# Performance work log

Hardware: AMD Instinct MI355X
Metric: run time of the kernel (lower is better)

## Reference

```python
import jax, jax.numpy as jnp
import numpy as np

RATIO, DS = 0.4, 4.0  # resolution, downsample_rate
B_, L_, C_, H_, W_ = 2, 4, 128, 96, 96


def get_transformation_matrix(M, H, W):
    # kornia-style rotation about image center: T = shift @ R @ shift_inv, then add translation
    R = M[..., :2, :2]
    center = jnp.array([W / 2.0, H / 2.0], jnp.float32)
    t = center - jnp.einsum('...ij,j->...i', R, center) + M[..., :, 2]
    return jnp.concatenate([R, t[..., None]], axis=-1)  # (...,2,3)


def _grid_sample(img, grid):
    # img (N,C,H,W), grid (N,H,W,2) normalized; bilinear, zeros padding, align_corners=True
    N, C, H, W = img.shape
    gx = (grid[..., 0] + 1.0) * 0.5 * (W - 1)
    gy = (grid[..., 1] + 1.0) * 0.5 * (H - 1)
    x0 = jnp.floor(gx); y0 = jnp.floor(gy)
    wx = gx - x0; wy = gy - y0

    def one(im, x0, y0, wx, wy):
        def samp(xi, yi):
            valid = ((xi >= 0) & (xi <= W - 1) & (yi >= 0) & (yi <= H - 1)).astype(im.dtype)
            xc = jnp.clip(xi, 0, W - 1).astype(jnp.int32)
            yc = jnp.clip(yi, 0, H - 1).astype(jnp.int32)
            return im[:, yc, xc] * valid[None]
        return (samp(x0, y0) * (1 - wx) * (1 - wy) + samp(x0 + 1, y0) * wx * (1 - wy)
                + samp(x0, y0 + 1) * (1 - wx) * wy + samp(x0 + 1, y0 + 1) * wx * wy)

    return jax.vmap(one)(img, x0, y0, wx, wy)


def warp_affine(src, M, H, W):
    # torch F.affine_grid + grid_sample with normalized homography (align_corners=True)
    n = jnp.array([[2.0 / (W - 1), 0.0, -1.0],
                   [0.0, 2.0 / (H - 1), -1.0],
                   [0.0, 0.0, 1.0]], jnp.float32)
    bottom = jnp.broadcast_to(jnp.array([[0.0, 0.0, 1.0]], jnp.float32), M.shape[:-2] + (1, 3))
    Mh = jnp.concatenate([M, bottom], axis=-2)
    theta = jnp.linalg.inv(n @ Mh @ jnp.linalg.inv(n))[..., :2, :]
    xs = jnp.linspace(-1.0, 1.0, W); ys = jnp.linspace(-1.0, 1.0, H)
    gx, gy = jnp.meshgrid(xs, ys)  # (H,W)
    pts = jnp.stack([gx, gy, jnp.ones_like(gx)], -1)
    grid = jnp.einsum('nij,hwj->nhwi', theta, pts)
    return _grid_sample(src, grid)


def _forward(x, record_len, pairwise_t_matrix, w1, b1, s1, t1, w2, b2, s2, t2,
             w3, b3, s3, t3, w4, b4, mlp_w, mlp_b):
    _, C, H, W = x.shape
    B, L = pairwise_t_matrix.shape[:2]
    N = L  # regular grouping: record_len[b] == L for all b
    feats = x.reshape(B, N, C, H, W)

    # get_discretized_transformation_matrix: rows [0,1], cols [0,1,3]; translation / (ratio*ds)
    tm = pairwise_t_matrix[..., :2, :][..., jnp.array([0, 1, 3])]  # (B,L,L,2,3)
    tm = jnp.concatenate([tm[..., :2], tm[..., 2:] / (RATIO * DS)], axis=-1)

    # get_rotated_roi: warp all-ones maps by the pairwise transforms
    roi = warp_affine(jnp.ones((B * L * L, 1, H, W), x.dtype),
                      get_transformation_matrix(tm.reshape(-1, 2, 3), H, W), H, W)
    roi = roi.reshape(B, L, L, 1, H, W)

    # rearrange 'b c h w -> b c w h' then flip last axis
    f = jnp.flip(jnp.swapaxes(feats, -1, -2), axis=-1)  # (B,N,C,H,W), H==W
    is_first = jnp.zeros((B, N), bool).at[0, 0].set(True)  # first_frame flag -> (b=0,i=0)
    ch = jnp.arange(C)

    def pwf(h):
        # PixelWeightedFusionSoftmax trunk: 1x1 convs + inference BN (folded scale/shift) + relu
        def layer(h, w, b, s, t):
            h = jnp.einsum('nchw,oc->nohw', h, w) + b[:, None, None]
            return jax.nn.relu(h * s[:, None, None] + t[:, None, None])
        h = layer(h, w1, b1, s1, t1)
        h = layer(h, w2, b2, s2, t2)
        h = layer(h, w3, b3, s3, t3)
        return jax.nn.relu(jnp.einsum('nchw,oc->nohw', h, w4) + b4[:, None, None])  # (N,1,H,W)

    def per_target(f_b, tm_i, roi_i, ego_f, first):
        # f_b (N,C,H,W); tm_i (N,2,3); roi_i (N,1,H,W); ego_f (C,H,W)
        T = get_transformation_matrix(tm_i, H, W)
        neighbor = warp_affine(f_b, T, H, W)               # (N,C,H,W)
        ego = jnp.broadcast_to(ego_f[None], neighbor.shape)
        # process_features: replace top-k (k=1; k=C for the very first pair) std channels
        std = jnp.std(ego_f, axis=(1, 2), ddof=1)          # per-channel std (unbiased)
        chan_mask = (ch == jnp.argmax(std))[None, :, None, None]
        sel = jnp.where(first, neighbor, jnp.where(chan_mask, neighbor, ego))
        logits = pwf(jnp.concatenate([sel, ego], axis=1))  # (N,1,H,W)
        logits = jnp.where(roi_i == 0, -jnp.inf, logits)
        wgt = jax.nn.softmax(logits, axis=0)               # softmax over agents
        out = (wgt * sel * roi_i).sum(0)                   # (C,H,W)
        return jnp.swapaxes(jnp.flip(out, axis=-1), -1, -2)  # undo flip + rearrange

    def per_batch(f_b, tm_b, roi_b, first_b):
        return jax.vmap(per_target, in_axes=(None, 1, 1, 0, 0))(f_b, tm_b, roi_b, f_b, first_b)

    updated = jax.vmap(per_batch)(f, tm, roi, is_first)    # (B,N,C,H,W)
    out = jnp.transpose(updated[:, 0], (0, 2, 3, 1))       # ego agent, (B,H,W,C)
    return out @ mlp_w.T + mlp_b


def setup_inputs() -> dict:
    key = jax.random.key(0)
    ks = jax.random.split(key, 20)
    B, L, C, H, W = B_, L_, C_, H_, W_
    x = jax.random.normal(ks[0], (B * L, C, H, W), jnp.float32)
    record_len = jnp.full((B,), L, jnp.int32)

    # near-identity SE(2) pairwise transforms (exact identity on diagonal)
    ang = jax.random.uniform(ks[1], (B, L, L), minval=-0.1, maxval=0.1)
    tr = jax.random.uniform(ks[2], (B, L, L, 2), minval=-2.0, maxval=2.0)
    eye = jnp.eye(L, dtype=bool)[None]
    ang = jnp.where(eye, 0.0, ang)
    tr = jnp.where(eye[..., None], 0.0, tr)
    c, s = jnp.cos(ang), jnp.sin(ang)
    P = jnp.zeros((B, L, L, 4, 4), jnp.float32)
    P = P.at[..., 0, 0].set(c).at[..., 0, 1].set(-s).at[..., 1, 0].set(s).at[..., 1, 1].set(c)
    P = P.at[..., 2, 2].set(1.0).at[..., 3, 3].set(1.0)
    P = P.at[..., 0, 3].set(tr[..., 0]).at[..., 1, 3].set(tr[..., 1])

    def winit(k, o, i):
        return jax.random.normal(k, (o, i), jnp.float32) / np.sqrt(i).astype(np.float32)

    inp = dict(x=x, record_len=record_len, pairwise_t_matrix=P,
               w1=winit(ks[3], 128, 2 * C), b1=jnp.zeros(128, jnp.float32),
               s1=1.0 + 0.1 * jax.random.normal(ks[4], (128,), jnp.float32),
               t1=0.1 * jax.random.normal(ks[5], (128,), jnp.float32),
               w2=winit(ks[6], 32, 128), b2=jnp.zeros(32, jnp.float32),
               s2=1.0 + 0.1 * jax.random.normal(ks[7], (32,), jnp.float32),
               t2=0.1 * jax.random.normal(ks[8], (32,), jnp.float32),
               w3=winit(ks[9], 8, 32), b3=jnp.zeros(8, jnp.float32),
               s3=1.0 + 0.1 * jax.random.normal(ks[10], (8,), jnp.float32),
               t3=0.1 * jax.random.normal(ks[11], (8,), jnp.float32),
               w4=winit(ks[12], 1, 8), b4=jnp.zeros(1, jnp.float32),
               mlp_w=winit(ks[13], C, C),
               mlp_b=0.01 * jax.random.normal(ks[14], (C,), jnp.float32))
    return inp


def reference(x, record_len, pairwise_t_matrix, w1, b1, s1, t1, w2, b2, s2, t2,
              w3, b3, s3, t3, w4, b4, mlp_w, mlp_b):
    return _forward(x, record_len, pairwise_t_matrix, w1, b1, s1, t1, w2, b2, s2, t2,
                    w3, b3, s3, t3, w4, b4, mlp_w, mlp_b)
```

## Files before the change

kernel.cpp:

```cpp
#include <hip/hip_runtime.h>
#include <hip/hip_bf16.h>
#include <math.h>

#define HW 9216
#define CC 128

typedef __attribute__((ext_vector_type(4))) float f32x4;
typedef __attribute__((ext_vector_type(8))) short s16x8;

static __device__ __forceinline__ unsigned short f2bf(float f) {
    __hip_bfloat16 h = __float2bfloat16(f);
    return *reinterpret_cast<unsigned short*>(&h);
}
static __device__ __forceinline__ float bf2f(unsigned short u) {
    unsigned int v = ((unsigned int)u) << 16;
    float f;
    __builtin_memcpy(&f, &v, 4);
    return f;
}

__global__ void k_theta(const float* __restrict__ P, float* __restrict__ th) {
    int t = threadIdx.x;
    if (t >= 8) return;
    int b = t >> 2, j = t & 3;
    const float* M = P + (size_t)(b * 4 + j) * 64;
    float a00 = M[0], a01 = M[1], a02 = M[3] / 1.6f;
    float a10 = M[4], a11 = M[5], a12 = M[7] / 1.6f;
    const float cx = 48.f, cy = 48.f;
    float T02 = cx - (a00 * cx + a01 * cy) + a02;
    float T12 = cy - (a10 * cx + a11 * cy) + a12;
    float A02 = a00 + a01 - 1.f + (2.f / 95.f) * T02;
    float A12 = a10 + a11 - 1.f + (2.f / 95.f) * T12;
    float det = a00 * a11 - a01 * a10;
    float i00 = a11 / det, i01 = -a01 / det, i10 = -a10 / det, i11 = a00 / det;
    float* o = th + t * 6;
    o[0] = i00; o[1] = i01; o[2] = -(i00 * A02 + i01 * A12);
    o[3] = i10; o[4] = i11; o[5] = -(i10 * A02 + i11 * A12);
}

__global__ __launch_bounds__(256) void k_wcvt(const float* __restrict__ w1, const float* __restrict__ w2,
                                              const float* __restrict__ mw,
                                              unsigned short* __restrict__ w1b, unsigned short* __restrict__ w2b,
                                              unsigned short* __restrict__ mwb) {
    int t = blockIdx.x * 256 + threadIdx.x;
    int nthr = gridDim.x * 256;
    for (int i = t; i < 32768; i += nthr) w1b[i] = f2bf(w1[i]);
    for (int i = t; i < 16384; i += nthr) mwb[i] = f2bf(mw[i]);
    if (t < 4096) w2b[t] = f2bf(w2[t]);
}

__global__ __launch_bounds__(256) void k_transpose(const float* __restrict__ x, unsigned short* __restrict__ xT) {
    int bn = blockIdx.x / 96, y = blockIdx.x % 96;
    __shared__ float tile[96][129];
    const float* src = x + (size_t)bn * 128 * HW + (size_t)y * 96;
    for (int i = threadIdx.x; i < 128 * 96; i += 256) {
        int c = i / 96, xx = i - c * 96;
        tile[xx][c] = src[(size_t)c * HW + xx];
    }
    __syncthreads();
    unsigned int* dst = (unsigned int*)(xT + ((size_t)bn * 96 + y) * 96 * 128);
    for (int i = threadIdx.x; i < 96 * 64; i += 256) {
        int xx = i >> 6, cp = i & 63;
        unsigned int pk = (unsigned int)f2bf(tile[xx][cp * 2]) | ((unsigned int)f2bf(tile[xx][cp * 2 + 1]) << 16);
        dst[xx * 64 + cp] = pk;
    }
}

__global__ __launch_bounds__(256) void k_var(const float* __restrict__ x, float* __restrict__ var) {
    int b = blockIdx.x >> 7, c = blockIdx.x & 127;
    const float* src = x + ((size_t)(b * 4) * 128 + c) * HW;
    float s = 0.f, ss = 0.f;
    for (int i = threadIdx.x; i < HW; i += 256) { float v = src[i]; s += v; ss += v * v; }
    __shared__ float rs[256], rss[256];
    rs[threadIdx.x] = s; rss[threadIdx.x] = ss; __syncthreads();
    for (int o = 128; o > 0; o >>= 1) {
        if (threadIdx.x < o) { rs[threadIdx.x] += rs[threadIdx.x + o]; rss[threadIdx.x] += rss[threadIdx.x + o]; }
        __syncthreads();
    }
    if (threadIdx.x == 0) {
        float mean = rs[0] / 9216.f;
        var[b * 128 + c] = (rss[0] - 9216.f * mean * mean) / 9215.f;
    }
}

__global__ void k_argmax(const float* __restrict__ var, int* __restrict__ cmax) {
    int b = blockIdx.x, t = threadIdx.x;
    __shared__ float v[128]; __shared__ int idx[128];
    v[t] = var[b * 128 + t]; idx[t] = t; __syncthreads();
    for (int o = 64; o > 0; o >>= 1) {
        if (t < o) { if (v[t + o] > v[t]) { v[t] = v[t + o]; idx[t] = idx[t + o]; } }
        __syncthreads();
    }
    if (t == 0) cmax[b] = idx[0];
}

__global__ __launch_bounds__(256) void k_gather(const unsigned short* __restrict__ xT, const float* __restrict__ th,
                                                const int* __restrict__ cmax, unsigned short* __restrict__ sel16,
                                                float* __restrict__ roi) {
    int blk = blockIdx.x;
    int bj6 = blk / 576, pblk = blk - bj6 * 576;
    int b = bj6 / 3, jm = bj6 - b * 3, j = jm + 1;
    int pr = threadIdx.x >> 7, c = threadIdx.x & 127;
    const float* t6 = th + (b * 4 + j) * 6;
    float T0 = t6[0], T1 = t6[1], T2 = t6[2], T3 = t6[3], T4 = t6[4], T5 = t6[5];
    int cm = cmax[b];
    const unsigned short* base = xT + (size_t)(b * 4 + j) * HW * CC;
    const unsigned short* ebase = xT + (size_t)(b * 4) * HW * CC;
    #pragma unroll
    for (int it = 0; it < 8; it++) {
        int p = pblk * 16 + it * 2 + pr;
        int h = p / 96, w = p - h * 96;
        float X = -1.f + (2.f / 95.f) * (float)w, Y = -1.f + (2.f / 95.f) * (float)h;
        float gx = T0 * X + T1 * Y + T2;
        float gy = T3 * X + T4 * Y + T5;
        float px = (gx + 1.f) * 47.5f, py = (gy + 1.f) * 47.5f;
        float x0f = floorf(px), y0f = floorf(py);
        float wx = px - x0f, wy = py - y0f;
        int x0 = (int)x0f, y0 = (int)y0f, x1 = x0 + 1, y1 = y0 + 1;
        float w00 = (1.f - wx) * (1.f - wy), w10 = wx * (1.f - wy);
        float w01 = (1.f - wx) * wy, w11 = wx * wy;
        bool vx0 = (x0 >= 0) && (x0 <= 95), vx1 = (x1 >= 0) && (x1 <= 95);
        bool vy0 = (y0 >= 0) && (y0 <= 95), vy1 = (y1 >= 0) && (y1 <= 95);
        float f00 = (vx0 && vy0) ? w00 : 0.f, f10 = (vx1 && vy0) ? w10 : 0.f;
        float f01 = (vx0 && vy1) ? w01 : 0.f, f11 = (vx1 && vy1) ? w11 : 0.f;
        int xc0 = min(max(x0, 0), 95), xc1 = min(max(x1, 0), 95);
        int yc0 = min(max(y0, 0), 95), yc1 = min(max(y1, 0), 95);
        float nb = f00 * bf2f(base[((95 - xc0) * 96 + yc0) * CC + c])
                 + f10 * bf2f(base[((95 - xc1) * 96 + yc0) * CC + c])
                 + f01 * bf2f(base[((95 - xc0) * 96 + yc1) * CC + c])
                 + f11 * bf2f(base[((95 - xc1) * 96 + yc1) * CC + c]);
        unsigned short egov = ebase[((95 - w) * 96 + h) * CC + c];
        unsigned short sv = (b == 0) ? f2bf(nb) : ((c == cm) ? f2bf(nb) : egov);
        sel16[((size_t)bj6 * HW + p) * CC + c] = sv;
        if (c == 0) roi[(size_t)bj6 * HW + p] = f00 + f10 + f01 + f11;
    }
}

__global__ __launch_bounds__(256) void k_fused(
    const unsigned short* __restrict__ xT, const unsigned short* __restrict__ sel16,
    const float* __restrict__ roiB,
    const unsigned short* __restrict__ w1b, const unsigned short* __restrict__ w2b,
    const unsigned short* __restrict__ mwb,
    const float* __restrict__ b1, const float* __restrict__ s1, const float* __restrict__ t1,
    const float* __restrict__ b2, const float* __restrict__ s2, const float* __restrict__ t2,
    const float* __restrict__ w3, const float* __restrict__ b3, const float* __restrict__ s3,
    const float* __restrict__ t3, const float* __restrict__ w4, const float* __restrict__ b4,
    const float* __restrict__ mb, float* __restrict__ out) {
    __shared__ __align__(16) unsigned char sm[47232];
    float* l2s  = (float*)(sm + 40960);
    float* lgs  = (float*)(sm + 45696);
    float* rois = (float*)(sm + 46208);
    float* wgt  = (float*)(sm + 46720);
    int t = threadIdx.x;
    int blk = blockIdx.x;
    int b = blk / 288, pt = blk - b * 288;
    int p0 = pt * 32;
    const unsigned short* egb = xT + (size_t)(b * 4) * HW * CC;
    #pragma unroll
    for (int it = 0; it < 2; it++) {
        int u = it * 256 + t;
        int px = u >> 4, g = u & 15;
        int p = p0 + px;
        int h = p / 96, w = p - h * 96;
        s16x8 v = *(const s16x8*)(egb + (size_t)((95 - w) * 96 + h) * CC + g * 8);
        *(s16x8*)(sm + px * 256 + ((g * 16) ^ ((px & 7) << 4))) = v;
    }
    #pragma unroll
    for (int j = 1; j < 4; j++) {
        const unsigned short* sp = sel16 + ((size_t)(b * 3 + j - 1) * HW + p0) * CC;
        #pragma unroll
        for (int it = 0; it < 2; it++) {
            int u = it * 256 + t;
            int px = u >> 4, g = u & 15;
            s16x8 v = *(const s16x8*)(sp + px * 128 + g * 8);
            *(s16x8*)(sm + j * 8192 + px * 256 + ((g * 16) ^ ((px & 7) << 4))) = v;
        }
    }
    if (t < 128) {
        int j = t >> 5, px = t & 31;
        rois[j * 32 + px] = (j == 0) ? 1.f : roiB[(size_t)(b * 3 + j - 1) * HW + p0 + px];
    }
    int lane = t & 63, w_ = t >> 6, l15 = lane & 15, l4 = lane >> 4;
    float bb[2], ss[2], tt[2];
    #pragma unroll
    for (int nt = 0; nt < 2; nt++) {
        int o = w_ * 32 + nt * 16 + l15;
        bb[nt] = b1[o]; ss[nt] = s1[o]; tt[nt] = t1[o];
    }
    int mt2 = w_ >> 1, nt2 = w_ & 1;
    float b2v, s2v, t2v;
    { int o2 = nt2 * 16 + l15; b2v = b2[o2]; s2v = s2[o2]; t2v = t2[o2]; }
    __syncthreads();
    for (int j = 0; j < 4; j++) {
        f32x4 acc[2][2];
        #pragma unroll
        for (int mt = 0; mt < 2; mt++)
            #pragma unroll
            for (int nt = 0; nt < 2; nt++) acc[mt][nt] = f32x4{0.f, 0.f, 0.f, 0.f};
        const unsigned char* selj = sm + j * 8192;
        #pragma unroll
        for (int kt = 0; kt < 8; kt++) {
            const unsigned char* src = (kt < 4) ? selj : sm;
            int kloc = (kt & 3) * 32 + l4 * 8;
            s16x8 bfr[2];
            #pragma unroll
            for (int nt = 0; nt < 2; nt++)
                bfr[nt] = *(const s16x8*)(w1b + (size_t)(w_ * 32 + nt * 16 + l15) * 256 + kt * 32 + l4 * 8);
            #pragma unroll
            for (int mt = 0; mt < 2; mt++) {
                int px = mt * 16 + l15;
                s16x8 af = *(const s16x8*)(src + px * 256 + ((2 * kloc) ^ ((px & 7) << 4)));
                #pragma unroll
                for (int nt = 0; nt < 2; nt++)
                    acc[mt][nt] = __builtin_amdgcn_mfma_f32_16x16x32_bf16(af, bfr[nt], acc[mt][nt], 0, 0, 0);
            }
        }
        __syncthreads();
        #pragma unroll
        for (int mt = 0; mt < 2; mt++) {
            #pragma unroll
            for (int nt = 0; nt < 2; nt++) {
                int o = w_ * 32 + nt * 16 + l15;
                #pragma unroll
                for (int r = 0; r < 4; r++) {
                    int px = mt * 16 + l4 * 4 + r;
                    float v = fmaxf((acc[mt][nt][r] + bb[nt]) * ss[nt] + tt[nt], 0.f);
                    *(unsigned short*)(sm + 32768 + px * 256 + ((2 * o) ^ ((px & 7) << 4))) = f2bf(v);
                }
            }
        }
        __syncthreads();
        f32x4 acc2 = f32x4{0.f, 0.f, 0.f, 0.f};
        {
            int px = mt2 * 16 + l15;
            #pragma unroll
            for (int kt = 0; kt < 4; kt++) {
                s16x8 af = *(const s16x8*)(sm + 32768 + px * 256 + ((2 * (kt * 32 + l4 * 8)) ^ ((px & 7) << 4)));
                s16x8 bf = *(const s16x8*)(w2b + (size_t)(nt2 * 16 + l15) * 128 + kt * 32 + l4 * 8);
                acc2 = __builtin_amdgcn_mfma_f32_16x16x32_bf16(af, bf, acc2, 0, 0, 0);
            }
        }
        {
            int o2 = nt2 * 16 + l15;
            #pragma unroll
            for (int r = 0; r < 4; r++) {
                int pxr = mt2 * 16 + l4 * 4 + r;
                l2s[pxr * 37 + o2] = fmaxf((acc2[r] + b2v) * s2v + t2v, 0.f);
            }
        }
        __syncthreads();
        if (t < 32) {
            int px = t;
            float xv[32];
            #pragma unroll
            for (int k = 0; k < 32; k++) xv[k] = l2s[px * 37 + k];
            float lg = b4[0];
            #pragma unroll
            for (int o = 0; o < 8; o++) {
                float a = 0.f;
                #pragma unroll
                for (int k = 0; k < 32; k++) a += xv[k] * w3[o * 32 + k];
                float l3v = fmaxf((a + b3[o]) * s3[o] + t3[o], 0.f);
                lg += w4[o] * l3v;
            }
            lgs[j * 32 + px] = fmaxf(lg, 0.f);
        }
    }
    __syncthreads();
    if (t < 32) {
        int px = t;
        float rr[4], lg[4];
        #pragma unroll
        for (int j = 0; j < 4; j++) { rr[j] = rois[j * 32 + px]; lg[j] = lgs[j * 32 + px]; }
        float m = -1e30f;
        #pragma unroll
        for (int j = 0; j < 4; j++) if (rr[j] != 0.f && lg[j] > m) m = lg[j];
        float e[4], se = 0.f;
        #pragma unroll
        for (int j = 0; j < 4; j++) { e[j] = (rr[j] != 0.f) ? expf(lg[j] - m) : 0.f; se += e[j]; }
        float inv = 1.f / se;
        #pragma unroll
        for (int j = 0; j < 4; j++) wgt[j * 32 + px] = e[j] * inv * rr[j];
    }
    __syncthreads();
    #pragma unroll
    for (int it = 0; it < 2; it++) {
        int u = it * 256 + t;
        int px = u >> 4, g = u & 15;
        int byo = (g * 16) ^ ((px & 7) << 4);
        float wj[4];
        #pragma unroll
        for (int j = 0; j < 4; j++) wj[j] = wgt[j * 32 + px];
        float accv[8];
        #pragma unroll
        for (int e = 0; e < 8; e++) accv[e] = 0.f;
        #pragma unroll
        for (int j = 0; j < 4; j++) {
            s16x8 v = *(const s16x8*)(sm + j * 8192 + px * 256 + byo);
            #pragma unroll
            for (int e = 0; e < 8; e++) accv[e] += wj[j] * bf2f((unsigned short)v[e]);
        }
        s16x8 pk;
        #pragma unroll
        for (int e = 0; e < 8; e++) pk[e] = (short)f2bf(accv[e]);
        *(s16x8*)(sm + 32768 + px * 256 + byo) = pk;
    }
    __syncthreads();
    f32x4 acc3[2][2];
    #pragma unroll
    for (int mt = 0; mt < 2; mt++)
        #pragma unroll
        for (int nt = 0; nt < 2; nt++) acc3[mt][nt] = f32x4{0.f, 0.f, 0.f, 0.f};
    #pragma unroll
    for (int kt = 0; kt < 4; kt++) {
        s16x8 bfr[2];
        #pragma unroll
        for (int nt = 0; nt < 2; nt++)
            bfr[nt] = *(const s16x8*)(mwb + (size_t)(w_ * 32 + nt * 16 + l15) * 128 + kt * 32 + l4 * 8);
        #pragma unroll
        for (int mt = 0; mt < 2; mt++) {
            int px = mt * 16 + l15;
            s16x8 af = *(const s16x8*)(sm + 32768 + px * 256 + ((kt * 64 + l4 * 16) ^ ((px & 7) << 4)));
            #pragma unroll
            for (int nt = 0; nt < 2; nt++)
                acc3[mt][nt] = __builtin_amdgcn_mfma_f32_16x16x32_bf16(af, bfr[nt], acc3[mt][nt], 0, 0, 0);
        }
    }
    float mbv[2];
    #pragma unroll
    for (int nt = 0; nt < 2; nt++) mbv[nt] = mb[w_ * 32 + nt * 16 + l15];
    #pragma unroll
    for (int mt = 0; mt < 2; mt++) {
        #pragma unroll
        for (int nt = 0; nt < 2; nt++) {
            #pragma unroll
            for (int r = 0; r < 4; r++) {
                int px = mt * 16 + l4 * 4 + r;
                int p = p0 + px;
                int h = p / 96, ww = p - h * 96;
                out[(((size_t)b * 96 + (95 - ww)) * 96 + h) * CC + w_ * 32 + nt * 16 + l15] = acc3[mt][nt][r] + mbv[nt];
            }
        }
    }
}

extern "C" void kernel_launch(void* const* d_in, const int* in_sizes, int n_in,
                              void* d_out, int out_size, void* d_ws, size_t ws_size,
                              hipStream_t stream) {
    const float* x  = (const float*)d_in[0];
    const float* P  = (const float*)d_in[2];
    const float* w1 = (const float*)d_in[3];
    const float* b1 = (const float*)d_in[4];
    const float* s1 = (const float*)d_in[5];
    const float* t1 = (const float*)d_in[6];
    const float* w2 = (const float*)d_in[7];
    const float* b2 = (const float*)d_in[8];
    const float* s2 = (const float*)d_in[9];
    const float* t2 = (const float*)d_in[10];
    const float* w3 = (const float*)d_in[11];
    const float* b3 = (const float*)d_in[12];
    const float* s3 = (const float*)d_in[13];
    const float* t3 = (const float*)d_in[14];
    const float* w4 = (const float*)d_in[15];
    const float* b4 = (const float*)d_in[16];
    const float* mw = (const float*)d_in[17];
    const float* mb = (const float*)d_in[18];
    float* out = (float*)d_out;

    float* ws = (float*)d_ws;
    float* TH  = ws;
    float* VAR = ws + 64;
    int*   CMX = (int*)(ws + 320);
    unsigned short* XT    = (unsigned short*)(ws + 384);
    unsigned short* SEL16 = XT + 9437184;
    float* ROI = (float*)(SEL16 + 7077888);
    unsigned short* W1B = (unsigned short*)(ROI + 55296);
    unsigned short* W2B = W1B + 32768;
    unsigned short* MWB = W2B + 4096;

    k_theta<<<1, 64, 0, stream>>>(P, TH);
    k_wcvt<<<32, 256, 0, stream>>>(w1, w2, mw, W1B, W2B, MWB);
    k_transpose<<<768, 256, 0, stream>>>(x, XT);
    k_var<<<256, 256, 0, stream>>>(x, VAR);
    k_argmax<<<2, 128, 0, stream>>>(VAR, CMX);
    k_gather<<<3456, 256, 0, stream>>>(XT, TH, CMX, SEL16, ROI);
    k_fused<<<576, 256, 0, stream>>>(XT, SEL16, ROI, W1B, W2B, MWB,
                                     b1, s1, t1, b2, s2, t2, w3, b3, s3, t3, w4, b4, mb, out);
}
```

Measured before the change: 185.9 us.

## Fuse variance into transpose, vectorize gather, restructure fused MLP per-wave

Merges the theta and weight-conversion kernels into one prep kernel. The per-channel variance is now computed inside the transpose kernel from the shared tile, with atomics into a zeroed buffer, which removes a separate full read of x. The gather kernel now loads 8 channels per thread with 16-byte vector loads instead of scalar bf16 loads. The fused kernel gives each wave its own agent j, so it computes all 128 outputs with per-wave scratch and no block-wide barriers between stages, and the weighted-sum stage is folded into the final MFMA A-operand load; in exchange shared memory grows to about 66 KB, which may reduce occupancy.

```diff
diff --git a/kernel.cpp b/kernel.cpp
--- a/kernel.cpp
+++ b/kernel.cpp
@@ -19,37 +19,37 @@
     return f;
 }
 
-__global__ void k_theta(const float* __restrict__ P, float* __restrict__ th) {
-    int t = threadIdx.x;
-    if (t >= 8) return;
-    int b = t >> 2, j = t & 3;
-    const float* M = P + (size_t)(b * 4 + j) * 64;
-    float a00 = M[0], a01 = M[1], a02 = M[3] / 1.6f;
-    float a10 = M[4], a11 = M[5], a12 = M[7] / 1.6f;
-    const float cx = 48.f, cy = 48.f;
-    float T02 = cx - (a00 * cx + a01 * cy) + a02;
-    float T12 = cy - (a10 * cx + a11 * cy) + a12;
-    float A02 = a00 + a01 - 1.f + (2.f / 95.f) * T02;
-    float A12 = a10 + a11 - 1.f + (2.f / 95.f) * T12;
-    float det = a00 * a11 - a01 * a10;
-    float i00 = a11 / det, i01 = -a01 / det, i10 = -a10 / det, i11 = a00 / det;
-    float* o = th + t * 6;
-    o[0] = i00; o[1] = i01; o[2] = -(i00 * A02 + i01 * A12);
-    o[3] = i10; o[4] = i11; o[5] = -(i10 * A02 + i11 * A12);
-}
-
-__global__ __launch_bounds__(256) void k_wcvt(const float* __restrict__ w1, const float* __restrict__ w2,
+__global__ __launch_bounds__(256) void k_prep(const float* __restrict__ P,
+                                              const float* __restrict__ w1, const float* __restrict__ w2,
                                               const float* __restrict__ mw,
+                                              float* __restrict__ th,
                                               unsigned short* __restrict__ w1b, unsigned short* __restrict__ w2b,
                                               unsigned short* __restrict__ mwb) {
     int t = blockIdx.x * 256 + threadIdx.x;
+    if (blockIdx.x == 0 && threadIdx.x < 8) {
+        int i = threadIdx.x;
+        const float* M = P + (size_t)i * 64;
+        float a00 = M[0], a01 = M[1], a02 = M[3] / 1.6f;
+        float a10 = M[4], a11 = M[5], a12 = M[7] / 1.6f;
+        const float cx = 48.f, cy = 48.f;
+        float T02 = cx - (a00 * cx + a01 * cy) + a02;
+        float T12 = cy - (a10 * cx + a11 * cy) + a12;
+        float A02 = a00 + a01 - 1.f + (2.f / 95.f) * T02;
+        float A12 = a10 + a11 - 1.f + (2.f / 95.f) * T12;
+        float det = a00 * a11 - a01 * a10;
+        float i00 = a11 / det, i01 = -a01 / det, i10 = -a10 / det, i11 = a00 / det;
+        float* o = th + i * 6;
+        o[0] = i00; o[1] = i01; o[2] = -(i00 * A02 + i01 * A12);
+        o[3] = i10; o[4] = i11; o[5] = -(i10 * A02 + i11 * A12);
+    }
     int nthr = gridDim.x * 256;
     for (int i = t; i < 32768; i += nthr) w1b[i] = f2bf(w1[i]);
     for (int i = t; i < 16384; i += nthr) mwb[i] = f2bf(mw[i]);
-    if (t < 4096) w2b[t] = f2bf(w2[t]);
-}
-
-__global__ __launch_bounds__(256) void k_transpose(const float* __restrict__ x, unsigned short* __restrict__ xT) {
+    for (int i = t; i < 4096; i += nthr) w2b[i] = f2bf(w2[i]);
+}
+
+__global__ __launch_bounds__(256) void k_transpose(const float* __restrict__ x, unsigned short* __restrict__ xT,
+                                                   float* __restrict__ vsum) {
     int bn = blockIdx.x / 96, y = blockIdx.x % 96;
     __shared__ float tile[96][129];
     const float* src = x + (size_t)bn * 128 * HW + (size_t)y * 96;
@@ -64,29 +64,24 @@
         unsigned int pk = (unsigned int)f2bf(tile[xx][cp * 2]) | ((unsigned int)f2bf(tile[xx][cp * 2 + 1]) << 16);
         dst[xx * 64 + cp] = pk;
     }
-}
-
-__global__ __launch_bounds__(256) void k_var(const float* __restrict__ x, float* __restrict__ var) {
-    int b = blockIdx.x >> 7, c = blockIdx.x & 127;
-    const float* src = x + ((size_t)(b * 4) * 128 + c) * HW;
-    float s = 0.f, ss = 0.f;
-    for (int i = threadIdx.x; i < HW; i += 256) { float v = src[i]; s += v; ss += v * v; }
-    __shared__ float rs[256], rss[256];
-    rs[threadIdx.x] = s; rss[threadIdx.x] = ss; __syncthreads();
-    for (int o = 128; o > 0; o >>= 1) {
-        if (threadIdx.x < o) { rs[threadIdx.x] += rs[threadIdx.x + o]; rss[threadIdx.x] += rss[threadIdx.x + o]; }
-        __syncthreads();
-    }
-    if (threadIdx.x == 0) {
-        float mean = rs[0] / 9216.f;
-        var[b * 128 + c] = (rss[0] - 9216.f * mean * mean) / 9215.f;
-    }
-}
-
-__global__ void k_argmax(const float* __restrict__ var, int* __restrict__ cmax) {
+    if ((bn & 3) == 0 && threadIdx.x < 128) {
+        int c = threadIdx.x;
+        float s = 0.f, ss = 0.f;
+        #pragma unroll 8
+        for (int xx = 0; xx < 96; xx++) { float v = tile[xx][c]; s += v; ss += v * v; }
+        float* vp = vsum + (size_t)((bn >> 2) * 128 + c) * 2;
+        atomicAdd(vp, s);
+        atomicAdd(vp + 1, ss);
+    }
+}
+
+__global__ void k_argmax(const float* __restrict__ vsum, int* __restrict__ cmax) {
     int b = blockIdx.x, t = threadIdx.x;
     __shared__ float v[128]; __shared__ int idx[128];
-    v[t] = var[b * 128 + t]; idx[t] = t; __syncthreads();
+    float s = vsum[(b * 128 + t) * 2], ss = vsum[(b * 128 + t) * 2 + 1];
+    float mean = s / 9216.f;
+    v[t] = (ss - 9216.f * mean * mean) / 9215.f;
+    idx[t] = t; __syncthreads();
     for (int o = 64; o > 0; o >>= 1) {
         if (t < o) { if (v[t + o] > v[t]) { v[t] = v[t + o]; idx[t] = idx[t + o]; } }
         __syncthreads();
@@ -99,41 +94,46 @@
                                                 float* __restrict__ roi) {
     int blk = blockIdx.x;
     int bj6 = blk / 576, pblk = blk - bj6 * 576;
-    int b = bj6 / 3, jm = bj6 - b * 3, j = jm + 1;
-    int pr = threadIdx.x >> 7, c = threadIdx.x & 127;
+    int b = bj6 / 3, j = bj6 - b * 3 + 1;
+    int pxr = threadIdx.x >> 4, g = threadIdx.x & 15;
     const float* t6 = th + (b * 4 + j) * 6;
     float T0 = t6[0], T1 = t6[1], T2 = t6[2], T3 = t6[3], T4 = t6[4], T5 = t6[5];
     int cm = cmax[b];
     const unsigned short* base = xT + (size_t)(b * 4 + j) * HW * CC;
     const unsigned short* ebase = xT + (size_t)(b * 4) * HW * CC;
-    #pragma unroll
-    for (int it = 0; it < 8; it++) {
-        int p = pblk * 16 + it * 2 + pr;
-        int h = p / 96, w = p - h * 96;
-        float X = -1.f + (2.f / 95.f) * (float)w, Y = -1.f + (2.f / 95.f) * (float)h;
-        float gx = T0 * X + T1 * Y + T2;
-        float gy = T3 * X + T4 * Y + T5;
-        float px = (gx + 1.f) * 47.5f, py = (gy + 1.f) * 47.5f;
-        float x0f = floorf(px), y0f = floorf(py);
-        float wx = px - x0f, wy = py - y0f;
-        int x0 = (int)x0f, y0 = (int)y0f, x1 = x0 + 1, y1 = y0 + 1;
-        float w00 = (1.f - wx) * (1.f - wy), w10 = wx * (1.f - wy);
-        float w01 = (1.f - wx) * wy, w11 = wx * wy;
-        bool vx0 = (x0 >= 0) && (x0 <= 95), vx1 = (x1 >= 0) && (x1 <= 95);
-        bool vy0 = (y0 >= 0) && (y0 <= 95), vy1 = (y1 >= 0) && (y1 <= 95);
-        float f00 = (vx0 && vy0) ? w00 : 0.f, f10 = (vx1 && vy0) ? w10 : 0.f;
-        float f01 = (vx0 && vy1) ? w01 : 0.f, f11 = (vx1 && vy1) ? w11 : 0.f;
-        int xc0 = min(max(x0, 0), 95), xc1 = min(max(x1, 0), 95);
-        int yc0 = min(max(y0, 0), 95), yc1 = min(max(y1, 0), 95);
-        float nb = f00 * bf2f(base[((95 - xc0) * 96 + yc0) * CC + c])
-                 + f10 * bf2f(base[((95 - xc1) * 96 + yc0) * CC + c])
-                 + f01 * bf2f(base[((95 - xc0) * 96 + yc1) * CC + c])
-                 + f11 * bf2f(base[((95 - xc1) * 96 + yc1) * CC + c]);
-        unsigned short egov = ebase[((95 - w) * 96 + h) * CC + c];
-        unsigned short sv = (b == 0) ? f2bf(nb) : ((c == cm) ? f2bf(nb) : egov);
-        sel16[((size_t)bj6 * HW + p) * CC + c] = sv;
-        if (c == 0) roi[(size_t)bj6 * HW + p] = f00 + f10 + f01 + f11;
-    }
+    int p = pblk * 16 + pxr;
+    int h = p / 96, w = p - h * 96;
+    float X = -1.f + (2.f / 95.f) * (float)w, Y = -1.f + (2.f / 95.f) * (float)h;
+    float gx = T0 * X + T1 * Y + T2;
+    float gy = T3 * X + T4 * Y + T5;
+    float px = (gx + 1.f) * 47.5f, py = (gy + 1.f) * 47.5f;
+    float x0f = floorf(px), y0f = floorf(py);
+    float wx = px - x0f, wy = py - y0f;
+    int x0 = (int)x0f, y0 = (int)y0f, x1 = x0 + 1, y1 = y0 + 1;
+    float w00 = (1.f - wx) * (1.f - wy), w10 = wx * (1.f - wy);
+    float w01 = (1.f - wx) * wy, w11 = wx * wy;
+    bool vx0 = (x0 >= 0) && (x0 <= 95), vx1 = (x1 >= 0) && (x1 <= 95);
+    bool vy0 = (y0 >= 0) && (y0 <= 95), vy1 = (y1 >= 0) && (y1 <= 95);
+    float f00 = (vx0 && vy0) ? w00 : 0.f, f10 = (vx1 && vy0) ? w10 : 0.f;
+    float f01 = (vx0 && vy1) ? w01 : 0.f, f11 = (vx1 && vy1) ? w11 : 0.f;
+    int xc0 = min(max(x0, 0), 95), xc1 = min(max(x1, 0), 95);
+    int yc0 = min(max(y0, 0), 95), yc1 = min(max(y1, 0), 95);
+    s16x8 v00 = *(const s16x8*)(base + (size_t)((95 - xc0) * 96 + yc0) * CC + g * 8);
+    s16x8 v10 = *(const s16x8*)(base + (size_t)((95 - xc1) * 96 + yc0) * CC + g * 8);
+    s16x8 v01 = *(const s16x8*)(base + (size_t)((95 - xc0) * 96 + yc1) * CC + g * 8);
+    s16x8 v11 = *(const s16x8*)(base + (size_t)((95 - xc1) * 96 + yc1) * CC + g * 8);
+    s16x8 ve  = *(const s16x8*)(ebase + (size_t)((95 - w) * 96 + h) * CC + g * 8);
+    s16x8 sv;
+    #pragma unroll
+    for (int e = 0; e < 8; e++) {
+        float nb = f00 * bf2f((unsigned short)v00[e]) + f10 * bf2f((unsigned short)v10[e])
+                 + f01 * bf2f((unsigned short)v01[e]) + f11 * bf2f((unsigned short)v11[e]);
+        int c = g * 8 + e;
+        unsigned short r = (b == 0) ? f2bf(nb) : ((c == cm) ? f2bf(nb) : (unsigned short)ve[e]);
+        sv[e] = (short)r;
+    }
+    *(s16x8*)(sel16 + ((size_t)bj6 * HW + p) * CC + g * 8) = sv;
+    if (g == 0) roi[(size_t)bj6 * HW + p] = f00 + f10 + f01 + f11;
 }
 
 __global__ __launch_bounds__(256) void k_fused(
@@ -146,11 +146,11 @@
     const float* __restrict__ w3, const float* __restrict__ b3, const float* __restrict__ s3,
     const float* __restrict__ t3, const float* __restrict__ w4, const float* __restrict__ b4,
     const float* __restrict__ mb, float* __restrict__ out) {
-    __shared__ __align__(16) unsigned char sm[47232];
-    float* l2s  = (float*)(sm + 40960);
-    float* lgs  = (float*)(sm + 45696);
-    float* rois = (float*)(sm + 46208);
-    float* wgt  = (float*)(sm + 46720);
+    __shared__ __align__(16) unsigned char sm[67840];
+    float* lgs  = (float*)(sm + 65536);
+    float* rois = (float*)(sm + 66048);
+    float* w3s  = (float*)(sm + 66560);
+    float* cs3  = (float*)(sm + 67712);
     int t = threadIdx.x;
     int blk = blockIdx.x;
     int b = blk / 288, pt = blk - b * 288;
@@ -180,95 +180,109 @@
         int j = t >> 5, px = t & 31;
         rois[j * 32 + px] = (j == 0) ? 1.f : roiB[(size_t)(b * 3 + j - 1) * HW + p0 + px];
     }
+    { int o = t >> 5, k = t & 31; w3s[o * 36 + k] = w3[o * 32 + k]; }
+    if (t < 8) { cs3[t] = b3[t]; cs3[8 + t] = s3[t]; cs3[16 + t] = t3[t]; cs3[24 + t] = w4[t]; }
     int lane = t & 63, w_ = t >> 6, l15 = lane & 15, l4 = lane >> 4;
-    float bb[2], ss[2], tt[2];
+    unsigned char* scratch = sm + 32768 + w_ * 8192;
+    __syncthreads();
+    f32x4 acc[2][8];
+    #pragma unroll
+    for (int mt = 0; mt < 2; mt++)
+        #pragma unroll
+        for (int nt = 0; nt < 8; nt++) acc[mt][nt] = f32x4{0.f, 0.f, 0.f, 0.f};
+    const unsigned char* tj = sm + w_ * 8192;
+    #pragma unroll
+    for (int kt = 0; kt < 8; kt++) {
+        const unsigned char* asrc = (kt < 4) ? tj : sm;
+        int kb = (kt & 3) * 64 + l4 * 16;
+        s16x8 af[2];
+        #pragma unroll
+        for (int mt = 0; mt < 2; mt++)
+            af[mt] = *(const s16x8*)(asrc + (mt * 16 + l15) * 256 + (kb ^ ((l15 & 7) << 4)));
+        #pragma unroll
+        for (int nt = 0; nt < 8; nt++) {
+            s16x8 bf = *(const s16x8*)(w1b + (size_t)(nt * 16 + l15) * 256 + kt * 32 + l4 * 8);
+            #pragma unroll
+            for (int mt = 0; mt < 2; mt++)
+                acc[mt][nt] = __builtin_amdgcn_mfma_f32_16x16x32_bf16(af[mt], bf, acc[mt][nt], 0, 0, 0);
+        }
+    }
+    #pragma unroll
+    for (int nt = 0; nt < 8; nt++) {
+        int o = nt * 16 + l15;
+        float bb = b1[o], sv = s1[o], tv = t1[o];
+        #pragma unroll
+        for (int mt = 0; mt < 2; mt++) {
+            #pragma unroll
+            for (int r = 0; r < 4; r++) {
+                int px = mt * 16 + l4 * 4 + r;
+                float v = fmaxf((acc[mt][nt][r] + bb) * sv + tv, 0.f);
+                *(unsigned short*)(scratch + px * 256 + ((2 * o) ^ ((px & 7) << 4))) = f2bf(v);
+            }
+        }
+    }
+    asm volatile("s_waitcnt lgkmcnt(0)" ::: "memory");
+    f32x4 acc2[2][2];
+    #pragma unroll
+    for (int mt = 0; mt < 2; mt++)
+        #pragma unroll
+        for (int nt = 0; nt < 2; nt++) acc2[mt][nt] = f32x4{0.f, 0.f, 0.f, 0.f};
+    #pragma unroll
+    for (int kt = 0; kt < 4; kt++) {
+        s16x8 af2[2];
+        #pragma unroll
+        for (int mt = 0; mt < 2; mt++) {
+            int px = mt * 16 + l15;
+            af2[mt] = *(const s16x8*)(scratch + px * 256 + ((2 * (kt * 32 + l4 * 8)) ^ ((px & 7) << 4)));
+        }
+        #pragma unroll
+        for (int nt = 0; nt < 2; nt++) {
+            s16x8 bf = *(const s16x8*)(w2b + (size_t)(nt * 16 + l15) * 128 + kt * 32 + l4 * 8);
+            #pragma unroll
+            for (int mt = 0; mt < 2; mt++)
+                acc2[mt][nt] = __builtin_amdgcn_mfma_f32_16x16x32_bf16(af2[mt], bf, acc2[mt][nt], 0, 0, 0);
+        }
+    }
+    asm volatile("s_waitcnt lgkmcnt(0)" ::: "memory");
+    float* l2s = (float*)scratch;
     #pragma unroll
     for (int nt = 0; nt < 2; nt++) {
-        int o = w_ * 32 + nt * 16 + l15;
-        bb[nt] = b1[o]; ss[nt] = s1[o]; tt[nt] = t1[o];
-    }
-    int mt2 = w_ >> 1, nt2 = w_ & 1;
-    float b2v, s2v, t2v;
-    { int o2 = nt2 * 16 + l15; b2v = b2[o2]; s2v = s2[o2]; t2v = t2[o2]; }
+        int o = nt * 16 + l15;
+        float bb = b2[o], sv = s2[o], tv = t2[o];
+        #pragma unroll
+        for (int mt = 0; mt < 2; mt++) {
+            #pragma unroll
+            for (int r = 0; r < 4; r++) {
+                int px = mt * 16 + l4 * 4 + r;
+                l2s[px * 36 + o] = fmaxf((acc2[mt][nt][r] + bb) * sv + tv, 0.f);
+            }
+        }
+    }
+    asm volatile("s_waitcnt lgkmcnt(0)" ::: "memory");
+    if (lane < 32) {
+        int px = lane;
+        f32x4 xv[8];
+        #pragma unroll
+        for (int kc = 0; kc < 8; kc++) xv[kc] = *(const f32x4*)(l2s + px * 36 + kc * 4);
+        float lg = b4[0];
+        #pragma unroll
+        for (int o = 0; o < 8; o++) {
+            float a = 0.f;
+            #pragma unroll
+            for (int kc = 0; kc < 8; kc++) {
+                f32x4 wv = *(const f32x4*)(w3s + o * 36 + kc * 4);
+                a += xv[kc][0] * wv[0] + xv[kc][1] * wv[1] + xv[kc][2] * wv[2] + xv[kc][3] * wv[3];
+            }
+            float l3 = fmaxf((a + cs3[o]) * cs3[8 + o] + cs3[16 + o], 0.f);
+            lg += cs3[24 + o] * l3;
+        }
+        lgs[w_ * 32 + px] = fmaxf(lg, 0.f);
+    }
     __syncthreads();
-    for (int j = 0; j < 4; j++) {
-        f32x4 acc[2][2];
-        #pragma unroll
-        for (int mt = 0; mt < 2; mt++)
-            #pragma unroll
-            for (int nt = 0; nt < 2; nt++) acc[mt][nt] = f32x4{0.f, 0.f, 0.f, 0.f};
-        const unsigned char* selj = sm + j * 8192;
-        #pragma unroll
-        for (int kt = 0; kt < 8; kt++) {
-            const unsigned char* src = (kt < 4) ? selj : sm;
-            int kloc = (kt & 3) * 32 + l4 * 8;
-            s16x8 bfr[2];
-            #pragma unroll
-            for (int nt = 0; nt < 2; nt++)
-                bfr[nt] = *(const s16x8*)(w1b + (size_t)(w_ * 32 + nt * 16 + l15) * 256 + kt * 32 + l4 * 8);
-            #pragma unroll
-            for (int mt = 0; mt < 2; mt++) {
-                int px = mt * 16 + l15;
-                s16x8 af = *(const s16x8*)(src + px * 256 + ((2 * kloc) ^ ((px & 7) << 4)));
-                #pragma unroll
-                for (int nt = 0; nt < 2; nt++)
-                    acc[mt][nt] = __builtin_amdgcn_mfma_f32_16x16x32_bf16(af, bfr[nt], acc[mt][nt], 0, 0, 0);
-            }
-        }
-        __syncthreads();
-        #pragma unroll
-        for (int mt = 0; mt < 2; mt++) {
-            #pragma unroll
-            for (int nt = 0; nt < 2; nt++) {
-                int o = w_ * 32 + nt * 16 + l15;
-                #pragma unroll
-                for (int r = 0; r < 4; r++) {
-                    int px = mt * 16 + l4 * 4 + r;
-                    float v = fmaxf((acc[mt][nt][r] + bb[nt]) * ss[nt] + tt[nt], 0.f);
-                    *(unsigned short*)(sm + 32768 + px * 256 + ((2 * o) ^ ((px & 7) << 4))) = f2bf(v);
-                }
-            }
-        }
-        __syncthreads();
-        f32x4 acc2 = f32x4{0.f, 0.f, 0.f, 0.f};
-        {
-            int px = mt2 * 16 + l15;
-            #pragma unroll
-            for (int kt = 0; kt < 4; kt++) {
-                s16x8 af = *(const s16x8*)(sm + 32768 + px * 256 + ((2 * (kt * 32 + l4 * 8)) ^ ((px & 7) << 4)));
-                s16x8 bf = *(const s16x8*)(w2b + (size_t)(nt2 * 16 + l15) * 128 + kt * 32 + l4 * 8);
-                acc2 = __builtin_amdgcn_mfma_f32_16x16x32_bf16(af, bf, acc2, 0, 0, 0);
-            }
-        }
-        {
-            int o2 = nt2 * 16 + l15;
-            #pragma unroll
-            for (int r = 0; r < 4; r++) {
-                int pxr = mt2 * 16 + l4 * 4 + r;
-                l2s[pxr * 37 + o2] = fmaxf((acc2[r] + b2v) * s2v + t2v, 0.f);
-            }
-        }
-        __syncthreads();
-        if (t < 32) {
-            int px = t;
-            float xv[32];
-            #pragma unroll
-            for (int k = 0; k < 32; k++) xv[k] = l2s[px * 37 + k];
-            float lg = b4[0];
-            #pragma unroll
-            for (int o = 0; o < 8; o++) {
-                float a = 0.f;
-                #pragma unroll
-                for (int k = 0; k < 32; k++) a += xv[k] * w3[o * 32 + k];
-                float l3v = fmaxf((a + b3[o]) * s3[o] + t3[o], 0.f);
-                lg += w4[o] * l3v;
-            }
-            lgs[j * 32 + px] = fmaxf(lg, 0.f);
-        }
-    }
-    __syncthreads();
-    if (t < 32) {
-        int px = t;
+    float wgt[2][4];
+    #pragma unroll
+    for (int mt = 0; mt < 2; mt++) {
+        int px = mt * 16 + l15;
         float rr[4], lg[4];
         #pragma unroll
         for (int j = 0; j < 4; j++) { rr[j] = rois[j * 32 + px]; lg[j] = lgs[j * 32 + px]; }
@@ -280,32 +294,8 @@
         for (int j = 0; j < 4; j++) { e[j] = (rr[j] != 0.f) ? expf(lg[j] - m) : 0.f; se += e[j]; }
         float inv = 1.f / se;
         #pragma unroll
-        for (int j = 0; j < 4; j++) wgt[j * 32 + px] = e[j] * inv * rr[j];
-    }
-    __syncthreads();
-    #pragma unroll
-    for (int it = 0; it < 2; it++) {
-        int u = it * 256 + t;
-        int px = u >> 4, g = u & 15;
-        int byo = (g * 16) ^ ((px & 7) << 4);
-        float wj[4];
-        #pragma unroll
-        for (int j = 0; j < 4; j++) wj[j] = wgt[j * 32 + px];
-        float accv[8];
-        #pragma unroll
-        for (int e = 0; e < 8; e++) accv[e] = 0.f;
-        #pragma unroll
-        for (int j = 0; j < 4; j++) {
-            s16x8 v = *(const s16x8*)(sm + j * 8192 + px * 256 + byo);
-            #pragma unroll
-            for (int e = 0; e < 8; e++) accv[e] += wj[j] * bf2f((unsigned short)v[e]);
-        }
-        s16x8 pk;
-        #pragma unroll
-        for (int e = 0; e < 8; e++) pk[e] = (short)f2bf(accv[e]);
-        *(s16x8*)(sm + 32768 + px * 256 + byo) = pk;
-    }
-    __syncthreads();
+        for (int j = 0; j < 4; j++) wgt[mt][j] = e[j] * inv * rr[j];
+    }
     f32x4 acc3[2][2];
     #pragma unroll
     for (int mt = 0; mt < 2; mt++)
@@ -320,7 +310,20 @@
         #pragma unroll
         for (int mt = 0; mt < 2; mt++) {
             int px = mt * 16 + l15;
-            s16x8 af = *(const s16x8*)(sm + 32768 + px * 256 + ((kt * 64 + l4 * 16) ^ ((px & 7) << 4)));
+            int byo = (kt * 64 + l4 * 16) ^ ((l15 & 7) << 4);
+            float accv[8];
+            #pragma unroll
+            for (int e = 0; e < 8; e++) accv[e] = 0.f;
+            #pragma unroll
+            for (int j = 0; j < 4; j++) {
+                s16x8 v = *(const s16x8*)(sm + j * 8192 + px * 256 + byo);
+                float wj = wgt[mt][j];
+                #pragma unroll
+                for (int e = 0; e < 8; e++) accv[e] += wj * bf2f((unsigned short)v[e]);
+            }
+            s16x8 af;
+            #pragma unroll
+            for (int e = 0; e < 8; e++) af[e] = (short)f2bf(accv[e]);
             #pragma unroll
             for (int nt = 0; nt < 2; nt++)
                 acc3[mt][nt] = __builtin_amdgcn_mfma_f32_16x16x32_bf16(af, bfr[nt], acc3[mt][nt], 0, 0, 0);
@@ -368,21 +371,20 @@
     float* out = (float*)d_out;
 
     float* ws = (float*)d_ws;
-    float* TH  = ws;
-    float* VAR = ws + 64;
-    int*   CMX = (int*)(ws + 320);
-    unsigned short* XT    = (unsigned short*)(ws + 384);
+    float* TH   = ws;
+    float* VSUM = ws + 64;
+    int*   CMX  = (int*)(ws + 576);
+    unsigned short* XT    = (unsigned short*)(ws + 1024);
     unsigned short* SEL16 = XT + 9437184;
     float* ROI = (float*)(SEL16 + 7077888);
     unsigned short* W1B = (unsigned short*)(ROI + 55296);
     unsigned short* W2B = W1B + 32768;
     unsigned short* MWB = W2B + 4096;
 
-    k_theta<<<1, 64, 0, stream>>>(P, TH);
-    k_wcvt<<<32, 256, 0, stream>>>(w1, w2, mw, W1B, W2B, MWB);
-    k_transpose<<<768, 256, 0, stream>>>(x, XT);
-    k_var<<<256, 256, 0, stream>>>(x, VAR);
-    k_argmax<<<2, 128, 0, stream>>>(VAR, CMX);
+    hipMemsetAsync(VSUM, 0, 512 * sizeof(float), stream);
+    k_prep<<<16, 256, 0, stream>>>(P, w1, w2, mw, TH, W1B, W2B, MWB);
+    k_transpose<<<768, 256, 0, stream>>>(x, XT, VSUM);
+    k_argmax<<<2, 128, 0, stream>>>(VSUM, CMX);
     k_gather<<<3456, 256, 0, stream>>>(XT, TH, CMX, SEL16, ROI);
     k_fused<<<576, 256, 0, stream>>>(XT, SEL16, ROI, W1B, W2B, MWB,
                                      b1, s1, t1, b2, s2, t2, w3, b3, s3, t3, w4, b4, mb, out);
```

Measured after the change: 184.3 us. Within noise of the previous version (-0.9%).
